# Kernel tuning notes

Hardware: AMD Instinct MI355X
Metric: run time of the kernel (lower is better)

## Reference

```python
import jax, jax.numpy as jnp
import numpy as np

SLOT_SIZE = 64
START_IDX = 0  # slot2idx['<start>']
STOP_IDX = 1   # slot2idx['<stop>']
NEG_INF = -10000.0


def setup_inputs() -> dict:
    key = jax.random.key(0)
    k1, k2 = jax.random.split(key)
    B, T, S = 512, 512, SLOT_SIZE
    logits = jax.random.normal(k1, (B, T, S), dtype=jnp.float32)
    masks = jnp.ones((B, T), dtype=jnp.float32)
    # nn.Parameter(torch.randn(S, S)) with START/STOP constraints from __init__
    transitions = jax.random.normal(k2, (S, S), dtype=jnp.float32)
    transitions = transitions.at[START_IDX, :].set(NEG_INF)
    transitions = transitions.at[:, STOP_IDX].set(NEG_INF)
    return {"logits": logits, "masks": masks, "transitions": transitions}


def reference(logits, masks, transitions):
    """Faithful CRF.forward == _viterbi_decode(logits, masks).

    Replicates the original quirks:
      - masks multiply only the emission feat (transitions are NOT masked
        inside the Viterbi recursion);
      - path_score is taken from the LAST next_tag's (next_tag = S-1)
        score vector at the final timestep, and the backtrace is seeded
        from that same column's argmax;
      - the backtrace re-applies the last backpointer table once before
        walking backwards (exactly as the torch loop does), and the
        popped start tag is dropped, giving a (B, T-1) path.
    """
    B, T, S = logits.shape
    init = jnp.full((B, S), NEG_INF, dtype=logits.dtype).at[:, START_IDX].set(0.0)

    # masked emissions for timesteps 1..T-1, time-major for scan: (T-1, B, S)
    feats = jnp.swapaxes(logits[:, 1:, :] * masks[:, 1:, None], 0, 1)

    def step(fv, feat_t):
        # scores[b, next, prev] = fv[b, prev] + transitions[next, prev]
        scores = fv[:, None, :] + transitions[None, :, :]  # (B, S, S)
        bptr = jnp.argmax(scores, axis=2).astype(jnp.int32)  # (B, S)
        vmax = jnp.max(scores, axis=2)                       # (B, S)
        return vmax + feat_t, (bptr, vmax)

    _, (bptrs, vmaxs) = jax.lax.scan(step, init, feats)  # (T-1, B, S) each

    # torch quirk: next_tag_var / best_tag_id left over from next_tag = S-1
    path_score = vmaxs[-1][:, S - 1]          # (B,)
    t0 = bptrs[-1][:, S - 1]                  # (B,) seed for backtrace

    def back(tag, bp):
        new_tag = jnp.take_along_axis(bp, tag[:, None], axis=1)[:, 0]
        return new_tag, tag  # emit the tag BEFORE following the pointer

    # reverse scan walks bptrs from last to first; emitted ys land at their
    # original time index, so ys == reversed best_path (start tag dropped
    # because the final carry -- the start tag -- is never emitted).
    _, ys = jax.lax.scan(back, t0, bptrs, reverse=True)  # (T-1, B)
    best_seq = jnp.swapaxes(ys, 0, 1)  # (B, T-1)
    return path_score, best_seq
```

## Files before the change

### kernel.cpp

```cpp
#include <hip/hip_runtime.h>


constexpr int Bz = 512;
constexpr int Tz = 512;
constexpr int Sz = 64;
constexpr float NEGINF = -10000.0f;

__device__ __forceinline__ float rlf(float x, int lane) {
    return __int_as_float(__builtin_amdgcn_readlane(__float_as_int(x), lane));
}

__device__ __forceinline__ void lds_barrier() {
    asm volatile("s_waitcnt lgkmcnt(0)\n\ts_barrier" ::: "memory");
}

__global__ __launch_bounds__(256)
void crf_viterbi_kernel(const float* __restrict__ logits,
                        const float* __restrict__ masks,
                        const float* __restrict__ trans,
                        float* __restrict__ out)
{
    const int n  = threadIdx.x & 63;
    const int w  = __builtin_amdgcn_readfirstlane(threadIdx.x >> 6);
    const int b  = blockIdx.x;
    const int pb = 16 * w;
    const int tg = n ^ pb;

    __shared__ unsigned bp[128 * 64];
    __shared__ float pval[2][4][64];
    __shared__ int   pidx[2][4][64];
    __shared__ float ys[Tz - 1];

    float tr[16];
    {
        const float4* tr4 = reinterpret_cast<const float4*>(trans + tg * 64 + pb);
        #pragma unroll
        for (int k = 0; k < 4; ++k) {
            float4 t = tr4[k];
            tr[4 * k + 0] = t.x; tr[4 * k + 1] = t.y;
            tr[4 * k + 2] = t.z; tr[4 * k + 3] = t.w;
        }
    }

    float fv = (tg == 0) ? 0.0f : NEGINF;

    const float* lgbase = logits + (size_t)b * Tz * Sz;
    const float* mkbase = masks + (size_t)b * Tz;

    float lgc[4], lgn[4], mkc[4], mkn[4];
    #pragma unroll
    for (int k = 0; k < 4; ++k) {
        lgc[k] = lgbase[(1 + k) * Sz + tg];
        mkc[k] = mkbase[1 + k];
        lgn[k] = lgbase[(5 + k) * Sz + tg];
        mkn[k] = mkbase[5 + k];
    }

    unsigned pk = 0;
    float psc = 0.0f;

    auto step = [&](int k, float lg, float mk) {
        const int buf = k & 1;
        float v[16];
        #pragma unroll
        for (int j = 0; j < 16; ++j)
            v[j] = rlf(fv, j) + tr[j];

        float mv[8]; int mi[8];
        #pragma unroll
        for (int c = 0; c < 8; ++c) {
            bool g = v[2 * c + 1] > v[2 * c];
            mv[c] = g ? v[2 * c + 1] : v[2 * c];
            mi[c] = g ? (2 * c + 1) : (2 * c);
        }
        #pragma unroll
        for (int st = 1; st < 8; st <<= 1) {
            #pragma unroll
            for (int c = 0; c < 8; c += 2 * st) {
                bool g = mv[c + st] > mv[c];
                mv[c] = g ? mv[c + st] : mv[c];
                mi[c] = g ? mi[c + st] : mi[c];
            }
        }
        pval[buf][w][tg] = mv[0];
        pidx[buf][w][tg] = pb + mi[0];

        lds_barrier();

        float c0 = pval[buf][0][tg], c1 = pval[buf][1][tg];
        float c2 = pval[buf][2][tg], c3 = pval[buf][3][tg];
        int   j0 = pidx[buf][0][tg], j1 = pidx[buf][1][tg];
        int   j2 = pidx[buf][2][tg], j3 = pidx[buf][3][tg];
        bool g1 = c1 > c0;  float m01 = g1 ? c1 : c0;  int k01 = g1 ? j1 : j0;
        bool g3 = c3 > c2;  float m23 = g3 ? c3 : c2;  int k23 = g3 ? j3 : j2;
        bool gm = m23 > m01;
        float m  = gm ? m23 : m01;
        int   gi = gm ? k23 : k01;

        pk |= ((unsigned)gi) << (8 * k);
        fv = m + lg * mk;
        return m;
    };

    for (int g = 0; g < 127; ++g) {
        step(0, lgc[0], mkc[0]);
        step(1, lgc[1], mkc[1]);
        step(2, lgc[2], mkc[2]);
        step(3, lgc[3], mkc[3]);

        if (w == 0) bp[g * 64 + n] = pk;
        pk = 0;

        #pragma unroll
        for (int k = 0; k < 4; ++k) { lgc[k] = lgn[k]; mkc[k] = mkn[k]; }
        #pragma unroll
        for (int k = 0; k < 4; ++k) {
            int t = 4 * g + 9 + k;
            t = (t < Tz) ? t : (Tz - 1);
            lgn[k] = lgbase[t * Sz + tg];
            mkn[k] = mkbase[t];
        }
    }

    step(0, lgc[0], mkc[0]);
    step(1, lgc[1], mkc[1]);
    float mlast = step(2, lgc[2], mkc[2]);
    psc = mlast;

    if (w == 0) {
        bp[127 * 64 + n] = pk;
        if (n == 63) out[b] = psc;
    }
    __syncthreads();

    if (w == 0) {
        unsigned wcur = bp[127 * 64 + n];
        int w127_63 = __builtin_amdgcn_readlane((int)wcur, 63);
        int tag = (w127_63 >> 16) & 255;

        for (int g = 127; g >= 0; --g) {
            unsigned wnext = (g > 0) ? bp[(g - 1) * 64 + n] : 0u;
            int smax = (g == 127) ? 2 : 3;
            for (int s = smax; s >= 0; --s) {
                int idx = 4 * g + s;
                if (n == 0) ys[idx] = (float)tag;
                int wd = __builtin_amdgcn_readlane((int)wcur, tag);
                tag = (wd >> (8 * s)) & 255;
            }
            wcur = wnext;
        }
    }
    __syncthreads();

    float* outseq = out + Bz + (size_t)b * (Tz - 1);
    for (int k = threadIdx.x; k < Tz - 1; k += 256) outseq[k] = ys[k];
}

extern "C" void kernel_launch(void* const* d_in, const int* in_sizes, int n_in,
                              void* d_out, int out_size, void* d_ws, size_t ws_size,
                              hipStream_t stream) {
    const float* logits = (const float*)d_in[0];
    const float* masks  = (const float*)d_in[1];
    const float* trans  = (const float*)d_in[2];
    float* out = (float*)d_out;
    (void)in_sizes; (void)n_in; (void)out_size; (void)d_ws; (void)ws_size;

    crf_viterbi_kernel<<<dim3(Bz), dim3(256), 0, stream>>>(logits, masks, trans, out);
}
```

Measured before the change: 334.6 us.

## Process two batch rows per block with interleaved Viterbi recursions

Each 256-thread block now runs the Viterbi forward pass for two batch elements at once, and the grid is halved. Both recursions share each per-step LDS barrier and the transition registers, and their independent max/argmax chains give extra instruction-level parallelism inside each wave. Waves 0 and 1 each pack backpointers and run the backtrace for one of the two rows in parallel. The cost is doubled LDS use and register pressure per block, with fewer blocks to spread across CUs.

```diff
diff --git a/kernel.cpp b/kernel.cpp
--- a/kernel.cpp
+++ b/kernel.cpp
@@ -22,14 +22,16 @@
 {
     const int n  = threadIdx.x & 63;
     const int w  = __builtin_amdgcn_readfirstlane(threadIdx.x >> 6);
-    const int b  = blockIdx.x;
+    const int b0 = 2 * blockIdx.x;
+    const int b1 = 2 * blockIdx.x + 1;
     const int pb = 16 * w;
     const int tg = n ^ pb;
 
-    __shared__ unsigned bp[128 * 64];
-    __shared__ float pval[2][4][64];
-    __shared__ int   pidx[2][4][64];
-    __shared__ float ys[Tz - 1];
+    __shared__ unsigned bpA[128 * 64];
+    __shared__ unsigned bpB[128 * 64];
+    __shared__ float pvalA[2][4][64], pvalB[2][4][64];
+    __shared__ int   pidxA[2][4][64], pidxB[2][4][64];
+    __shared__ float ysA[Tz - 1], ysB[Tz - 1];
 
     float tr[16];
     {
@@ -42,30 +44,32 @@
         }
     }
 
-    float fv = (tg == 0) ? 0.0f : NEGINF;
-
-    const float* lgbase = logits + (size_t)b * Tz * Sz;
-    const float* mkbase = masks + (size_t)b * Tz;
-
-    float lgc[4], lgn[4], mkc[4], mkn[4];
+    float fvA = (tg == 0) ? 0.0f : NEGINF;
+    float fvB = fvA;
+
+    const float* lgbaseA = logits + (size_t)b0 * Tz * Sz;
+    const float* lgbaseB = logits + (size_t)b1 * Tz * Sz;
+    const float* mkbaseA = masks + (size_t)b0 * Tz;
+    const float* mkbaseB = masks + (size_t)b1 * Tz;
+
+    float lgcA[4], lgnA[4], mkcA[4], mknA[4];
+    float lgcB[4], lgnB[4], mkcB[4], mknB[4];
     #pragma unroll
     for (int k = 0; k < 4; ++k) {
-        lgc[k] = lgbase[(1 + k) * Sz + tg];
-        mkc[k] = mkbase[1 + k];
-        lgn[k] = lgbase[(5 + k) * Sz + tg];
-        mkn[k] = mkbase[5 + k];
-    }
-
-    unsigned pk = 0;
-    float psc = 0.0f;
-
-    auto step = [&](int k, float lg, float mk) {
-        const int buf = k & 1;
+        lgcA[k] = lgbaseA[(1 + k) * Sz + tg];  mkcA[k] = mkbaseA[1 + k];
+        lgnA[k] = lgbaseA[(5 + k) * Sz + tg];  mknA[k] = mkbaseA[5 + k];
+        lgcB[k] = lgbaseB[(1 + k) * Sz + tg];  mkcB[k] = mkbaseB[1 + k];
+        lgnB[k] = lgbaseB[(5 + k) * Sz + tg];  mknB[k] = mkbaseB[5 + k];
+    }
+
+    unsigned pkA = 0, pkB = 0;
+    float pscA = 0.0f, pscB = 0.0f;
+
+    auto reduce16 = [&](float fv, float& mval, int& midx) {
         float v[16];
         #pragma unroll
         for (int j = 0; j < 16; ++j)
             v[j] = rlf(fv, j) + tr[j];
-
         float mv[8]; int mi[8];
         #pragma unroll
         for (int c = 0; c < 8; ++c) {
@@ -82,58 +86,98 @@
                 mi[c] = g ? mi[c + st] : mi[c];
             }
         }
-        pval[buf][w][tg] = mv[0];
-        pidx[buf][w][tg] = pb + mi[0];
+        mval = mv[0]; midx = pb + mi[0];
+    };
+
+    auto step = [&](int k, float lgA, float mkA, float lgB, float mkB,
+                    float& mAout, float& mBout) {
+        const int buf = k & 1;
+        float mvA, mvB; int miA, miB;
+        reduce16(fvA, mvA, miA);
+        reduce16(fvB, mvB, miB);
+        pvalA[buf][w][tg] = mvA;  pidxA[buf][w][tg] = miA;
+        pvalB[buf][w][tg] = mvB;  pidxB[buf][w][tg] = miB;
 
         lds_barrier();
 
-        float c0 = pval[buf][0][tg], c1 = pval[buf][1][tg];
-        float c2 = pval[buf][2][tg], c3 = pval[buf][3][tg];
-        int   j0 = pidx[buf][0][tg], j1 = pidx[buf][1][tg];
-        int   j2 = pidx[buf][2][tg], j3 = pidx[buf][3][tg];
-        bool g1 = c1 > c0;  float m01 = g1 ? c1 : c0;  int k01 = g1 ? j1 : j0;
-        bool g3 = c3 > c2;  float m23 = g3 ? c3 : c2;  int k23 = g3 ? j3 : j2;
-        bool gm = m23 > m01;
-        float m  = gm ? m23 : m01;
-        int   gi = gm ? k23 : k01;
-
-        pk |= ((unsigned)gi) << (8 * k);
-        fv = m + lg * mk;
-        return m;
+        float a0 = pvalA[buf][0][tg], a1 = pvalA[buf][1][tg];
+        float a2 = pvalA[buf][2][tg], a3 = pvalA[buf][3][tg];
+        float b0v = pvalB[buf][0][tg], b1v = pvalB[buf][1][tg];
+        float b2v = pvalB[buf][2][tg], b3v = pvalB[buf][3][tg];
+
+        bool ga1 = a1 > a0;   float am01 = ga1 ? a1 : a0;
+        bool ga3 = a3 > a2;   float am23 = ga3 ? a3 : a2;
+        bool gam = am23 > am01;
+        float mA = gam ? am23 : am01;
+
+        bool gb1 = b1v > b0v; float bm01 = gb1 ? b1v : b0v;
+        bool gb3 = b3v > b2v; float bm23 = gb3 ? b3v : b2v;
+        bool gbm = bm23 > bm01;
+        float mB = gbm ? bm23 : bm01;
+
+        if (w == 0) {
+            int j0 = pidxA[buf][0][tg], j1 = pidxA[buf][1][tg];
+            int j2 = pidxA[buf][2][tg], j3 = pidxA[buf][3][tg];
+            int k01 = ga1 ? j1 : j0;
+            int k23 = ga3 ? j3 : j2;
+            int gi  = gam ? k23 : k01;
+            pkA |= ((unsigned)gi) << (8 * k);
+        } else if (w == 1) {
+            int j0 = pidxB[buf][0][tg], j1 = pidxB[buf][1][tg];
+            int j2 = pidxB[buf][2][tg], j3 = pidxB[buf][3][tg];
+            int k01 = gb1 ? j1 : j0;
+            int k23 = gb3 ? j3 : j2;
+            int gi  = gbm ? k23 : k01;
+            pkB |= ((unsigned)gi) << (8 * k);
+        }
+
+        fvA = mA + lgA * mkA;
+        fvB = mB + lgB * mkB;
+        mAout = mA; mBout = mB;
     };
 
+    float mA, mB;
+
     for (int g = 0; g < 127; ++g) {
-        step(0, lgc[0], mkc[0]);
-        step(1, lgc[1], mkc[1]);
-        step(2, lgc[2], mkc[2]);
-        step(3, lgc[3], mkc[3]);
-
-        if (w == 0) bp[g * 64 + n] = pk;
-        pk = 0;
-
-        #pragma unroll
-        for (int k = 0; k < 4; ++k) { lgc[k] = lgn[k]; mkc[k] = mkn[k]; }
+        step(0, lgcA[0], mkcA[0], lgcB[0], mkcB[0], mA, mB);
+        step(1, lgcA[1], mkcA[1], lgcB[1], mkcB[1], mA, mB);
+        step(2, lgcA[2], mkcA[2], lgcB[2], mkcB[2], mA, mB);
+        step(3, lgcA[3], mkcA[3], lgcB[3], mkcB[3], mA, mB);
+
+        if (w == 0) bpA[g * 64 + n] = pkA;
+        if (w == 1) bpB[g * 64 + tg] = pkB;
+        pkA = 0; pkB = 0;
+
+        #pragma unroll
+        for (int k = 0; k < 4; ++k) {
+            lgcA[k] = lgnA[k]; mkcA[k] = mknA[k];
+            lgcB[k] = lgnB[k]; mkcB[k] = mknB[k];
+        }
         #pragma unroll
         for (int k = 0; k < 4; ++k) {
             int t = 4 * g + 9 + k;
             t = (t < Tz) ? t : (Tz - 1);
-            lgn[k] = lgbase[t * Sz + tg];
-            mkn[k] = mkbase[t];
-        }
-    }
-
-    step(0, lgc[0], mkc[0]);
-    step(1, lgc[1], mkc[1]);
-    float mlast = step(2, lgc[2], mkc[2]);
-    psc = mlast;
+            lgnA[k] = lgbaseA[t * Sz + tg];  mknA[k] = mkbaseA[t];
+            lgnB[k] = lgbaseB[t * Sz + tg];  mknB[k] = mkbaseB[t];
+        }
+    }
+
+    step(0, lgcA[0], mkcA[0], lgcB[0], mkcB[0], mA, mB);
+    step(1, lgcA[1], mkcA[1], lgcB[1], mkcB[1], mA, mB);
+    step(2, lgcA[2], mkcA[2], lgcB[2], mkcB[2], mA, mB);
+    pscA = mA; pscB = mB;
 
     if (w == 0) {
-        bp[127 * 64 + n] = pk;
-        if (n == 63) out[b] = psc;
-    }
+        bpA[127 * 64 + n] = pkA;
+        if (n == 63) { out[b0] = pscA; out[b1] = pscB; }
+    }
+    if (w == 1) bpB[127 * 64 + tg] = pkB;
     __syncthreads();
 
-    if (w == 0) {
+    if (w < 2) {
+        const unsigned* bp = (w == 0) ? bpA : bpB;
+        float* ys = (w == 0) ? ysA : ysB;
+
         unsigned wcur = bp[127 * 64 + n];
         int w127_63 = __builtin_amdgcn_readlane((int)wcur, 63);
         int tag = (w127_63 >> 16) & 255;
@@ -152,8 +196,12 @@
     }
     __syncthreads();
 
-    float* outseq = out + Bz + (size_t)b * (Tz - 1);
-    for (int k = threadIdx.x; k < Tz - 1; k += 256) outseq[k] = ys[k];
+    float* outA = out + Bz + (size_t)b0 * (Tz - 1);
+    float* outB = out + Bz + (size_t)b1 * (Tz - 1);
+    for (int k = threadIdx.x; k < Tz - 1; k += 256) {
+        outA[k] = ysA[k];
+        outB[k] = ysB[k];
+    }
 }
 
 extern "C" void kernel_launch(void* const* d_in, const int* in_sizes, int n_in,
@@ -165,5 +213,5 @@
     float* out = (float*)d_out;
     (void)in_sizes; (void)n_in; (void)out_size; (void)d_ws; (void)ws_size;
 
-    crf_viterbi_kernel<<<dim3(Bz), dim3(256), 0, stream>>>(logits, masks, trans, out);
-}
+    crf_viterbi_kernel<<<dim3(Bz / 2), dim3(256), 0, stream>>>(logits, masks, trans, out);
+}
```

Measured after the change: 485.9 us. 45.2% more time.

## Split Viterbi max-reduction across two waves instead of four

Applied to the files above, without the earlier changes.

Each block now uses 128 threads (2 waves). Each wave covers 32 previous tags instead of 16, so it does 32 readlane+add steps and a 5-level argmax tree per timestep. The cross-wave combine shrinks to one LDS value/index pair per wave, and the per-step barrier spans only two waves. This aims to cut synchronization and LDS traffic on the serial recursion, at the cost of a longer per-wave dependency chain and more registers.

```diff
diff --git a/kernel.cpp b/kernel.cpp
--- a/kernel.cpp
+++ b/kernel.cpp
@@ -14,7 +14,7 @@
     asm volatile("s_waitcnt lgkmcnt(0)\n\ts_barrier" ::: "memory");
 }
 
-__global__ __launch_bounds__(256)
+__global__ __launch_bounds__(128)
 void crf_viterbi_kernel(const float* __restrict__ logits,
                         const float* __restrict__ masks,
                         const float* __restrict__ trans,
@@ -23,19 +23,19 @@
     const int n  = threadIdx.x & 63;
     const int w  = __builtin_amdgcn_readfirstlane(threadIdx.x >> 6);
     const int b  = blockIdx.x;
-    const int pb = 16 * w;
+    const int pb = 32 * w;
     const int tg = n ^ pb;
 
     __shared__ unsigned bp[128 * 64];
-    __shared__ float pval[2][4][64];
-    __shared__ int   pidx[2][4][64];
+    __shared__ float pval[2][2][64];
+    __shared__ int   pidx[2][2][64];
     __shared__ float ys[Tz - 1];
 
-    float tr[16];
+    float tr[32];
     {
         const float4* tr4 = reinterpret_cast<const float4*>(trans + tg * 64 + pb);
         #pragma unroll
-        for (int k = 0; k < 4; ++k) {
+        for (int k = 0; k < 8; ++k) {
             float4 t = tr4[k];
             tr[4 * k + 0] = t.x; tr[4 * k + 1] = t.y;
             tr[4 * k + 2] = t.z; tr[4 * k + 3] = t.w;
@@ -50,52 +50,50 @@
     float lgc[4], lgn[4], mkc[4], mkn[4];
     #pragma unroll
     for (int k = 0; k < 4; ++k) {
-        lgc[k] = lgbase[(1 + k) * Sz + tg];
-        mkc[k] = mkbase[1 + k];
-        lgn[k] = lgbase[(5 + k) * Sz + tg];
-        mkn[k] = mkbase[5 + k];
+        lgc[k] = lgbase[(1 + k) * Sz + tg];  mkc[k] = mkbase[1 + k];
+        lgn[k] = lgbase[(5 + k) * Sz + tg];  mkn[k] = mkbase[5 + k];
     }
 
     unsigned pk = 0;
     float psc = 0.0f;
 
-    auto step = [&](int k, float lg, float mk) {
+    auto step = [&](int k, float lg, float mk) -> float {
         const int buf = k & 1;
-        float v[16];
+        float mv[16]; int mi[16];
         #pragma unroll
-        for (int j = 0; j < 16; ++j)
-            v[j] = rlf(fv, j) + tr[j];
-
-        float mv[8]; int mi[8];
-        #pragma unroll
-        for (int c = 0; c < 8; ++c) {
-            bool g = v[2 * c + 1] > v[2 * c];
-            mv[c] = g ? v[2 * c + 1] : v[2 * c];
-            mi[c] = g ? (2 * c + 1) : (2 * c);
+        for (int c = 0; c < 16; ++c) {
+            float va = rlf(fv, 2 * c)     + tr[2 * c];
+            float vb = rlf(fv, 2 * c + 1) + tr[2 * c + 1];
+            bool g = vb > va;
+            mv[c] = g ? vb : va;
+            mi[c] = g ? (pb + 2 * c + 1) : (pb + 2 * c);
         }
         #pragma unroll
-        for (int st = 1; st < 8; st <<= 1) {
+        for (int st = 1; st < 16; st <<= 1) {
             #pragma unroll
-            for (int c = 0; c < 8; c += 2 * st) {
+            for (int c = 0; c < 16; c += 2 * st) {
                 bool g = mv[c + st] > mv[c];
                 mv[c] = g ? mv[c + st] : mv[c];
                 mi[c] = g ? mi[c + st] : mi[c];
             }
         }
+
         pval[buf][w][tg] = mv[0];
-        pidx[buf][w][tg] = pb + mi[0];
+        pidx[buf][w][tg] = pb + 0 * 0 + mi[0] - 0;
+        pidx[buf][w][tg] = mi[0];
 
         lds_barrier();
 
-        float c0 = pval[buf][0][tg], c1 = pval[buf][1][tg];
-        float c2 = pval[buf][2][tg], c3 = pval[buf][3][tg];
-        int   j0 = pidx[buf][0][tg], j1 = pidx[buf][1][tg];
-        int   j2 = pidx[buf][2][tg], j3 = pidx[buf][3][tg];
-        bool g1 = c1 > c0;  float m01 = g1 ? c1 : c0;  int k01 = g1 ? j1 : j0;
-        bool g3 = c3 > c2;  float m23 = g3 ? c3 : c2;  int k23 = g3 ? j3 : j2;
-        bool gm = m23 > m01;
-        float m  = gm ? m23 : m01;
-        int   gi = gm ? k23 : k01;
+        float ov = pval[buf][1 - w][tg];
+        int   oi = pidx[buf][1 - w][tg];
+
+        float lv = (w == 0) ? mv[0] : ov;
+        int   li = (w == 0) ? mi[0] : oi;
+        float rv = (w == 0) ? ov    : mv[0];
+        int   ri = (w == 0) ? oi    : mi[0];
+        bool g = rv > lv;
+        float m  = g ? rv : lv;
+        int   gi = g ? ri : li;
 
         pk |= ((unsigned)gi) << (8 * k);
         fv = m + lg * mk;
@@ -124,8 +122,7 @@
 
     step(0, lgc[0], mkc[0]);
     step(1, lgc[1], mkc[1]);
-    float mlast = step(2, lgc[2], mkc[2]);
-    psc = mlast;
+    psc = step(2, lgc[2], mkc[2]);
 
     if (w == 0) {
         bp[127 * 64 + n] = pk;
@@ -153,7 +150,7 @@
     __syncthreads();
 
     float* outseq = out + Bz + (size_t)b * (Tz - 1);
-    for (int k = threadIdx.x; k < Tz - 1; k += 256) outseq[k] = ys[k];
+    for (int k = threadIdx.x; k < Tz - 1; k += 128) outseq[k] = ys[k];
 }
 
 extern "C" void kernel_launch(void* const* d_in, const int* in_sizes, int n_in,
@@ -165,5 +162,5 @@
     float* out = (float*)d_out;
     (void)in_sizes; (void)n_in; (void)out_size; (void)d_ws; (void)ws_size;
 
-    crf_viterbi_kernel<<<dim3(Bz), dim3(256), 0, stream>>>(logits, masks, trans, out);
+    crf_viterbi_kernel<<<dim3(Bz), dim3(128), 0, stream>>>(logits, masks, trans, out);
 }
```

After: 455.1 us. +36.0%, slower.
